# Kernel tuning notes

Hardware: AMD Instinct MI355X
Metric: run time of the kernel (lower is better)

The kernel has to match this reference:

```python
import jax, jax.numpy as jnp
import numpy as np

B, NS, D, H = 1024, 32, 1024, 4096
LN_EPS = 1e-5


def _layer_norm(x, g, b):
    mu = jnp.mean(x, axis=-1, keepdims=True)
    var = jnp.mean(jnp.square(x - mu), axis=-1, keepdims=True)
    return (x - mu) * jax.lax.rsqrt(var + LN_EPS) * g + b


def setup_inputs() -> dict:
    key = jax.random.key(0)
    ks = jax.random.split(key, 12)
    sc = 0.02
    inp = {
        "x": jax.random.normal(ks[0], (B, D), jnp.float32),
        "S": jax.random.normal(ks[1], (B, NS, D), jnp.float32),
        # route_mlp: Linear(2D, D) -> GELU -> Linear(D, NS)
        "w_r1": jax.random.normal(ks[2], (2 * D, D), jnp.float32) * sc,
        "b_r1": jnp.zeros((D,), jnp.float32),
        "w_r2": jax.random.normal(ks[3], (D, NS), jnp.float32) * sc,
        "b_r2": jnp.zeros((NS,), jnp.float32),
        # GRUCell(D, D): gates ordered [r, z, n] as in torch
        "w_ih": jax.random.normal(ks[4], (D, 3 * D), jnp.float32) * sc,
        "w_hh": jax.random.normal(ks[5], (D, 3 * D), jnp.float32) * sc,
        "b_ih": jnp.zeros((3 * D,), jnp.float32),
        "b_hh": jnp.zeros((3 * D,), jnp.float32),
        # slot_proj: Linear(D, D)
        "w_proj": jax.random.normal(ks[6], (D, D), jnp.float32) * sc,
        "b_proj": jnp.zeros((D,), jnp.float32),
        # ln1 / ffn / ln2
        "ln1_g": jnp.ones((D,), jnp.float32),
        "ln1_b": jnp.zeros((D,), jnp.float32),
        "w_f1": jax.random.normal(ks[7], (D, H), jnp.float32) * sc,
        "b_f1": jnp.zeros((H,), jnp.float32),
        "w_f2": jax.random.normal(ks[8], (H, D), jnp.float32) * sc,
        "b_f2": jnp.zeros((D,), jnp.float32),
        "ln2_g": jnp.ones((D,), jnp.float32),
        "ln2_b": jnp.zeros((D,), jnp.float32),
    }
    return inp


def reference(x, S, w_r1, b_r1, w_r2, b_r2, w_ih, w_hh, b_ih, b_hh,
              w_proj, b_proj, ln1_g, ln1_b, w_f1, b_f1, w_f2, b_f2,
              ln2_g, ln2_b):
    tau = 1.0
    # --- context-aware routing ---
    slot_mean = jnp.mean(S, axis=1)                     # [B, D]
    ctx = jnp.concatenate([x, slot_mean], axis=-1)      # [B, 2D]
    h_r = jax.nn.gelu(ctx @ w_r1 + b_r1, approximate=False)
    r_logits = h_r @ w_r2 + b_r2                        # [B, NS]
    alpha = jax.nn.softmax(r_logits / tau, axis=-1)     # [B, NS]

    # --- GRU slot update: input U = alpha * x broadcast over slots ---
    U = alpha[:, :, None] * x[:, None, :]               # [B, NS, D]
    gi = U @ w_ih + b_ih                                # [B, NS, 3D]
    gh = S @ w_hh + b_hh                                # [B, NS, 3D]
    gi_r, gi_z, gi_n = jnp.split(gi, 3, axis=-1)
    gh_r, gh_z, gh_n = jnp.split(gh, 3, axis=-1)
    r = jax.nn.sigmoid(gi_r + gh_r)
    z = jax.nn.sigmoid(gi_z + gh_z)
    n = jnp.tanh(gi_n + r * gh_n)
    S_new = (1.0 - z) * n + z * S                       # [B, NS, D]

    # --- weighted readout (slot_dropout = 0.0) ---
    slot_context = jnp.sum(alpha[:, :, None] * S_new, axis=1)  # [B, D]
    slot_update = slot_context @ w_proj + b_proj
    x_mid = x + slot_update

    # --- FFN + residual + LayerNorms ---
    h = _layer_norm(x_mid, ln1_g, ln1_b)
    ff = jax.nn.gelu(h @ w_f1 + b_f1, approximate=False) @ w_f2 + b_f2
    x_out = _layer_norm(x_mid + ff, ln2_g, ln2_b)
    return (x_out, S_new, alpha)
```

## Files before the change

kernel.cpp:

```cpp
#include <hip/hip_runtime.h>
#include <hip/hip_bf16.h>

#define BB 1024
#define NSLOT 32
#define DD 1024
#define HH 4096

typedef __bf16 bfx8 __attribute__((ext_vector_type(8)));
typedef float f32x4 __attribute__((ext_vector_type(4)));

__device__ __forceinline__ unsigned short f2bfu(float f) {
  union { float f; unsigned u; } v; v.f = f;
  unsigned r = v.u + 0x7fffu + ((v.u >> 16) & 1u);
  return (unsigned short)(r >> 16);
}
__device__ __forceinline__ float bfu2f(unsigned short u) {
  union { unsigned u; float f; } v; v.u = ((unsigned)u) << 16; return v.f;
}
__device__ __forceinline__ float gelu_f(float x) {
  return 0.5f * x * (1.0f + erff(x * 0.70710678118654752f));
}

__device__ __forceinline__ float sigm_fast(float x) {
  return __builtin_amdgcn_rcpf(1.0f + __builtin_amdgcn_exp2f(-1.4426950408889634f * x));
}
__device__ __forceinline__ float tanh_fast(float x) {
  float t = __builtin_amdgcn_exp2f(2.8853900817779268f * x);
  return 1.0f - 2.0f * __builtin_amdgcn_rcpf(1.0f + t);
}

__device__ __forceinline__ void async16(const unsigned short* g, unsigned short* l) {
  __builtin_amdgcn_global_load_lds(
      (const __attribute__((address_space(1))) unsigned int*)g,
      (__attribute__((address_space(3))) unsigned int*)l, 16, 0, 0);
}


__global__ __launch_bounds__(256) void cvt_x_ctx(const float* __restrict__ x,
                                                 unsigned short* __restrict__ ctx) {
  int i = blockIdx.x * 256 + threadIdx.x;
  int b = i >> 8;
  int c4 = (i & 255) * 4;
  float4 v = ((const float4*)(x + (size_t)b * DD))[i & 255];
  ushort4 o; o.x = f2bfu(v.x); o.y = f2bfu(v.y); o.z = f2bfu(v.z); o.w = f2bfu(v.w);
  *(ushort4*)&ctx[(size_t)b * (2 * DD) + c4] = o;
}

__global__ __launch_bounds__(256) void cvt4(const float* __restrict__ in,
                                            unsigned short* __restrict__ out, int n4) {
  int i = blockIdx.x * 256 + threadIdx.x;
  if (i >= n4) return;
  float4 v = ((const float4*)in)[i];
  ushort4 o; o.x = f2bfu(v.x); o.y = f2bfu(v.y); o.z = f2bfu(v.z); o.w = f2bfu(v.w);
  ((ushort4*)out)[i] = o;
}

__global__ __launch_bounds__(256) void slot_mean_k(const unsigned short* __restrict__ Sb,
                                                   unsigned short* __restrict__ ctx) {
  int i = blockIdx.x * 256 + threadIdx.x;
  int b = i >> 10, d = i & 1023;
  const unsigned short* p = Sb + (size_t)b * NSLOT * DD + d;
  float s = 0.f;
  #pragma unroll
  for (int sl = 0; sl < NSLOT; sl++) s += bfu2f(p[sl * DD]);
  ctx[(size_t)b * (2 * DD) + DD + d] = f2bfu(s * (1.0f / NSLOT));
}

__global__ __launch_bounds__(256) void transp(const float* __restrict__ in,
                                              unsigned short* __restrict__ out,
                                              int R, int C) {
  __shared__ float t[32][33];
  int tx = threadIdx.x & 31, ty = threadIdx.x >> 5;
  int c0 = blockIdx.x * 32, r0 = blockIdx.y * 32;
  #pragma unroll
  for (int i = 0; i < 4; i++) {
    int r = r0 + ty * 4 + i;
    t[ty * 4 + i][tx] = in[(size_t)r * C + c0 + tx];
  }
  __syncthreads();
  #pragma unroll
  for (int i = 0; i < 4; i++) {
    int c = c0 + ty * 4 + i;
    out[(size_t)c * R + r0 + tx] = f2bfu(t[tx][ty * 4 + i]);
  }
}

template <int EPI>
__global__ __launch_bounds__(256) void gemm_nt(
    const unsigned short* __restrict__ A, int lda,
    const unsigned short* __restrict__ Bt, int ldb, int K,
    const float* __restrict__ bias,
    const float* __restrict__ add, int ldadd,
    float* __restrict__ outF, unsigned short* __restrict__ outB, int ldout) {
  __shared__ __align__(16) unsigned short lA[2][128 * 32];
  __shared__ __align__(16) unsigned short lB[2][64 * 32];
  const int tid = threadIdx.x;
  const int wave = tid >> 6, lane = tid & 63;
  const int wr = wave >> 1, wc = wave & 1;
  const int q = lane >> 4, l15 = lane & 15;
  const int row0 = blockIdx.y * 128;
  const int col0 = blockIdx.x * 64;
  const int halfA = 128 * 32, halfB = 64 * 32;

  const int lr = lane >> 2, scn = lane & 3;
  const unsigned short* aSrc[2];
  unsigned short* aDst[2];
  #pragma unroll
  for (int j = 0; j < 2; j++) {
    int R0 = (2 * wave + j) * 16;
    int r = R0 + lr;
    int c = scn ^ ((r >> 1) & 3);
    aSrc[j] = A + (size_t)(row0 + r) * lda + c * 8;
    aDst[j] = &lA[0][R0 * 32];
  }
  const unsigned short* bSrc;
  unsigned short* bDst;
  {
    int R0 = wave * 16;
    int r = R0 + lr;
    int c = scn ^ ((r >> 1) & 3);
    bSrc = Bt + (size_t)(col0 + r) * ldb + c * 8;
    bDst = &lB[0][R0 * 32];
  }

  int offA[4];
  #pragma unroll
  for (int m = 0; m < 4; m++) {
    int r = wr * 64 + m * 16 + l15;
    offA[m] = r * 32 + (q ^ ((r >> 1) & 3)) * 8;
  }
  int offB[2];
  #pragma unroll
  for (int n = 0; n < 2; n++) {
    int r = wc * 32 + n * 16 + l15;
    offB[n] = r * 32 + (q ^ ((r >> 1) & 3)) * 8;
  }

  f32x4 acc[4][2];
  #pragma unroll
  for (int m = 0; m < 4; m++)
    #pragma unroll
    for (int n = 0; n < 2; n++) acc[m][n] = (f32x4){0.f, 0.f, 0.f, 0.f};

  const int iters = K >> 6;
  for (int it = 0; it < iters; it++) {
    #pragma unroll
    for (int j = 0; j < 2; j++) {
      async16(aSrc[j], aDst[j]);
      async16(aSrc[j] + 32, aDst[j] + halfA);
      aSrc[j] += 64;
    }
    async16(bSrc, bDst);
    async16(bSrc + 32, bDst + halfB);
    bSrc += 64;
    __syncthreads();
    #pragma unroll
    for (int h = 0; h < 2; h++) {
      bfx8 af[4];
      #pragma unroll
      for (int m = 0; m < 4; m++) af[m] = *(const bfx8*)&lA[h][offA[m]];
      bfx8 bf0 = *(const bfx8*)&lB[h][offB[0]];
      bfx8 bf1 = *(const bfx8*)&lB[h][offB[1]];
      #pragma unroll
      for (int m = 0; m < 4; m++) {
        acc[m][0] = __builtin_amdgcn_mfma_f32_16x16x32_bf16(af[m], bf0, acc[m][0], 0, 0, 0);
        acc[m][1] = __builtin_amdgcn_mfma_f32_16x16x32_bf16(af[m], bf1, acc[m][1], 0, 0, 0);
      }
    }
    __syncthreads();
  }

  #pragma unroll
  for (int m = 0; m < 4; m++) {
    #pragma unroll
    for (int n = 0; n < 2; n++) {
      int gr0 = row0 + wr * 64 + m * 16 + q * 4;
      int gc = col0 + wc * 32 + n * 16 + l15;
      #pragma unroll
      for (int i = 0; i < 4; i++) {
        int gr = gr0 + i;
        float v = acc[m][n][i];
        if (EPI == 0) {
          outF[(size_t)gr * ldout + gc] = v;
        } else if (EPI == 1) {
          float t = gelu_f(v + bias[gc]);
          outB[(size_t)gr * ldout + gc] = f2bfu(t);
        } else {
          outF[(size_t)gr * ldout + gc] = v + bias[gc] + add[(size_t)gr * ldadd + gc];
        }
      }
    }
  }
}

__global__ __launch_bounds__(256, 2) void gru_gemm(
    const unsigned short* __restrict__ Sb, const unsigned short* __restrict__ Whht,
    const float* __restrict__ alpha, const float* __restrict__ xw,
    const float* __restrict__ b_ih, const float* __restrict__ b_hh,
    const float* __restrict__ Sf, float* __restrict__ Snew,
    unsigned short* __restrict__ sc_b) {
  __shared__ __align__(16) unsigned short lA[2][2][128 * 32];
  __shared__ __align__(16) unsigned short lB[2][2][192 * 32];
  const int tid = threadIdx.x;
  const int wave = tid >> 6, lane = tid & 63;
  const int wr = wave >> 1, wc = wave & 1;
  const int q = lane >> 4, l15 = lane & 15;
  const int row0 = blockIdx.y * 128;
  const int col0 = blockIdx.x * 64;

  const int lr = lane >> 2, scn = lane & 3;
  const unsigned short* aSrc[2];
  int aOff[2];
  #pragma unroll
  for (int j = 0; j < 2; j++) {
    int R0 = (2 * wave + j) * 16;
    int r = R0 + lr;
    int c = scn ^ ((r >> 1) & 3);
    aSrc[j] = Sb + (size_t)(row0 + r) * DD + c * 8;
    aOff[j] = R0 * 32;
  }
  const unsigned short* bSrc[3];
  int bOff[3];
  #pragma unroll
  for (int j = 0; j < 3; j++) {
    int R0 = (3 * wave + j) * 16;
    int r = R0 + lr;
    int g = r >> 6, cr = r & 63;
    int c = scn ^ ((r >> 1) & 3);
    bSrc[j] = Whht + ((size_t)g * DD + col0 + cr) * DD + c * 8;
    bOff[j] = R0 * 32;
  }

  int offA[4];
  #pragma unroll
  for (int m = 0; m < 4; m++) {
    int r = wr * 64 + m * 16 + l15;
    offA[m] = r * 32 + (q ^ ((r >> 1) & 3)) * 8;
  }
  int offB[3][2];
  #pragma unroll
  for (int g = 0; g < 3; g++)
    #pragma unroll
    for (int n = 0; n < 2; n++) {
      int r = g * 64 + wc * 32 + n * 16 + l15;
      offB[g][n] = r * 32 + (q ^ ((r >> 1) & 3)) * 8;
    }

  f32x4 acc[3][4][2];
  #pragma unroll
  for (int g = 0; g < 3; g++)
    #pragma unroll
    for (int m = 0; m < 4; m++)
      #pragma unroll
      for (int n = 0; n < 2; n++) acc[g][m][n] = (f32x4){0.f, 0.f, 0.f, 0.f};

#define STAGE(BUF)                                                          \
  {                                                                         \
    _Pragma("unroll")                                                       \
    for (int j = 0; j < 2; j++) {                                           \
      async16(aSrc[j], &lA[BUF][0][aOff[j]]);                               \
      async16(aSrc[j] + 32, &lA[BUF][1][aOff[j]]);                          \
      aSrc[j] += 64;                                                        \
    }                                                                       \
    _Pragma("unroll")                                                       \
    for (int j = 0; j < 3; j++) {                                           \
      async16(bSrc[j], &lB[BUF][0][bOff[j]]);                               \
      async16(bSrc[j] + 32, &lB[BUF][1][bOff[j]]);                          \
      bSrc[j] += 64;                                                        \
    }                                                                       \
  }

#define COMPUTE(BUF)                                                        \
  {                                                                         \
    _Pragma("unroll")                                                       \
    for (int h = 0; h < 2; h++) {                                           \
      bfx8 af[4];                                                           \
      _Pragma("unroll")                                                     \
      for (int m = 0; m < 4; m++) af[m] = *(const bfx8*)&lA[BUF][h][offA[m]]; \
      _Pragma("unroll")                                                     \
      for (int g = 0; g < 3; g++) {                                         \
        bfx8 bf0 = *(const bfx8*)&lB[BUF][h][offB[g][0]];                   \
        bfx8 bf1 = *(const bfx8*)&lB[BUF][h][offB[g][1]];                   \
        _Pragma("unroll")                                                   \
        for (int m = 0; m < 4; m++) {                                       \
          acc[g][m][0] = __builtin_amdgcn_mfma_f32_16x16x32_bf16(af[m], bf0, acc[g][m][0], 0, 0, 0); \
          acc[g][m][1] = __builtin_amdgcn_mfma_f32_16x16x32_bf16(af[m], bf1, acc[g][m][1], 0, 0, 0); \
        }                                                                   \
      }                                                                     \
    }                                                                       \
  }

#define WAIT_VM10 asm volatile("s_waitcnt vmcnt(10)" ::: "memory")
#define WAIT_VM0  asm volatile("s_waitcnt vmcnt(0)" ::: "memory")
#define WAIT_LGKM asm volatile("s_waitcnt lgkmcnt(0)" ::: "memory")
#define BAR __builtin_amdgcn_s_barrier()

  STAGE(0);
  for (int t = 0; t < 8; t++) {
    STAGE(1);
    WAIT_VM10; BAR;
    COMPUTE(0);
    WAIT_LGKM; BAR;
    if (t < 7) {
      STAGE(0);
      WAIT_VM10;
    } else {
      WAIT_VM0;
    }
    BAR;
    COMPUTE(1);
    if (t < 7) { WAIT_LGKM; BAR; }
  }

#undef STAGE
#undef COMPUTE
#undef WAIT_VM10
#undef WAIT_VM0
#undef WAIT_LGKM
#undef BAR

  float sfv[4][2][4];
  float av[4][4];
  #pragma unroll
  for (int m = 0; m < 4; m++) {
    #pragma unroll
    for (int i = 0; i < 4; i++) {
      int gr = row0 + wr * 64 + m * 16 + q * 4 + i;
      av[m][i] = alpha[gr];
      const float* sfr = Sf + (size_t)gr * DD;
      #pragma unroll
      for (int n = 0; n < 2; n++)
        sfv[m][n][i] = sfr[col0 + wc * 32 + n * 16 + l15];
    }
  }

  float scp[2][2] = {{0.f, 0.f}, {0.f, 0.f}};
  #pragma unroll
  for (int m = 0; m < 4; m++) {
    #pragma unroll
    for (int i = 0; i < 4; i++) {
      int gr = row0 + wr * 64 + m * 16 + q * 4 + i;
      float a = av[m][i];
      const float* xwr = xw + (size_t)(gr >> 5) * (3 * DD);
      float* orow = Snew + (size_t)gr * DD;
      #pragma unroll
      for (int n = 0; n < 2; n++) {
        int gc = col0 + wc * 32 + n * 16 + l15;
        float ghr = acc[0][m][n][i] + b_hh[gc];
        float ghz = acc[1][m][n][i] + b_hh[gc + DD];
        float ghn = acc[2][m][n][i] + b_hh[gc + 2 * DD];
        float r = sigm_fast(a * xwr[gc] + b_ih[gc] + ghr);
        float z = sigm_fast(a * xwr[gc + DD] + b_ih[gc + DD] + ghz);
        float nn = tanh_fast(a * xwr[gc + 2 * DD] + b_ih[gc + 2 * DD] + r * ghn);
        float sv = (1.0f - z) * nn + z * sfv[m][n][i];
        orow[gc] = sv;
        scp[m >> 1][n] += a * sv;
      }
    }
  }
  #pragma unroll
  for (int bh = 0; bh < 2; bh++)
    #pragma unroll
    for (int n = 0; n < 2; n++) {
      float v = scp[bh][n];
      v += __shfl_xor(v, 16);
      v += __shfl_xor(v, 32);
      if (q == 0) {
        int batch = (row0 >> 5) + wr * 2 + bh;
        int gc = col0 + wc * 32 + n * 16 + l15;
        sc_b[(size_t)batch * DD + gc] = f2bfu(v);
      }
    }
}

__global__ __launch_bounds__(256) void route_softmax(
    const unsigned short* __restrict__ h_r, const float* __restrict__ w_r2,
    const float* __restrict__ b_r2, float* __restrict__ alpha_out) {
  int b = blockIdx.x;
  int n = threadIdx.x & 31, c = threadIdx.x >> 5;
  __shared__ float part[8][32];
  __shared__ float logits[32];
  const unsigned short* hr = h_r + (size_t)b * DD;
  float s = 0.f;
  for (int i = 0; i < 128; i++) {
    int k = c * 128 + i;
    s += bfu2f(hr[k]) * w_r2[k * NSLOT + n];
  }
  part[c][n] = s;
  __syncthreads();
  if (threadIdx.x < 32) {
    float t = b_r2[n];
    #pragma unroll
    for (int cc = 0; cc < 8; cc++) t += part[cc][n];
    logits[n] = t;
  }
  __syncthreads();
  if (threadIdx.x < 32) {
    float mx = -1e30f;
    #pragma unroll
    for (int j = 0; j < 32; j++) mx = fmaxf(mx, logits[j]);
    float den = 0.f;
    #pragma unroll
    for (int j = 0; j < 32; j++) den += expf(logits[j] - mx);
    alpha_out[(size_t)b * NSLOT + n] = expf(logits[n] - mx) / den;
  }
}

template <int OUT_BF>
__global__ __launch_bounds__(256) void ln_k(const float* __restrict__ in,
                                            const float* __restrict__ gw,
                                            const float* __restrict__ bw,
                                            float* __restrict__ outF,
                                            unsigned short* __restrict__ outB) {
  int b = blockIdx.x;
  int tid = threadIdx.x;
  float4 v = ((const float4*)(in + (size_t)b * DD))[tid];
  float s = v.x + v.y + v.z + v.w;
  float s2 = v.x * v.x + v.y * v.y + v.z * v.z + v.w * v.w;
  #pragma unroll
  for (int o = 32; o > 0; o >>= 1) { s += __shfl_down(s, o); s2 += __shfl_down(s2, o); }
  __shared__ float as1[4], as2[4];
  int wave = tid >> 6, lane = tid & 63;
  if (lane == 0) { as1[wave] = s; as2[wave] = s2; }
  __syncthreads();
  float t1 = as1[0] + as1[1] + as1[2] + as1[3];
  float t2 = as2[0] + as2[1] + as2[2] + as2[3];
  float mu = t1 * (1.0f / DD);
  float var = t2 * (1.0f / DD) - mu * mu;
  float rstd = rsqrtf(var + 1e-5f);
  int d = tid * 4;
  float o0 = (v.x - mu) * rstd * gw[d] + bw[d];
  float o1 = (v.y - mu) * rstd * gw[d + 1] + bw[d + 1];
  float o2 = (v.z - mu) * rstd * gw[d + 2] + bw[d + 2];
  float o3 = (v.w - mu) * rstd * gw[d + 3] + bw[d + 3];
  if (OUT_BF) {
    ushort4 o; o.x = f2bfu(o0); o.y = f2bfu(o1); o.z = f2bfu(o2); o.w = f2bfu(o3);
    *(ushort4*)&outB[(size_t)b * DD + d] = o;
  } else {
    float4 o; o.x = o0; o.y = o1; o.z = o2; o.w = o3;
    *(float4*)&outF[(size_t)b * DD + d] = o;
  }
}

extern "C" void kernel_launch(void* const* d_in, const int* in_sizes, int n_in,
                              void* d_out, int out_size, void* d_ws, size_t ws_size,
                              hipStream_t stream) {
  const float* x      = (const float*)d_in[0];
  const float* S      = (const float*)d_in[1];
  const float* w_r1   = (const float*)d_in[2];
  const float* b_r1   = (const float*)d_in[3];
  const float* w_r2   = (const float*)d_in[4];
  const float* b_r2   = (const float*)d_in[5];
  const float* w_ih   = (const float*)d_in[6];
  const float* w_hh   = (const float*)d_in[7];
  const float* b_ih   = (const float*)d_in[8];
  const float* b_hh   = (const float*)d_in[9];
  const float* w_proj = (const float*)d_in[10];
  const float* b_proj = (const float*)d_in[11];
  const float* ln1_g  = (const float*)d_in[12];
  const float* ln1_b  = (const float*)d_in[13];
  const float* w_f1   = (const float*)d_in[14];
  const float* b_f1   = (const float*)d_in[15];
  const float* w_f2   = (const float*)d_in[16];
  const float* b_f2   = (const float*)d_in[17];
  const float* ln2_g  = (const float*)d_in[18];
  const float* ln2_b  = (const float*)d_in[19];

  float* out_x = (float*)d_out;
  float* out_S = out_x + (size_t)BB * DD;
  float* out_a = out_S + (size_t)BB * NSLOT * DD;

  char* ws = (char*)d_ws;
  unsigned short* ctx    = (unsigned short*)(ws + 0);
  unsigned short* w_r1t  = (unsigned short*)(ws + 4194304);
  unsigned short* w_iht  = (unsigned short*)(ws + 8388608);
  unsigned short* w_hht  = (unsigned short*)(ws + 14680064);
  unsigned short* w_projt= (unsigned short*)(ws + 20971520);
  unsigned short* w_f1t  = (unsigned short*)(ws + 23068672);
  unsigned short* w_f2t  = (unsigned short*)(ws + 31457280);
  unsigned short* h_r    = (unsigned short*)(ws + 39845888);
  float*          xw     = (float*)(ws + 41943040);
  unsigned short* Sb     = (unsigned short*)(ws + 54525952);
  unsigned short* sc_b   = (unsigned short*)(ws + 0);
  float*          x_mid  = (float*)(ws + 41943040);
  unsigned short* h_ln   = (unsigned short*)(ws + 46137344);
  float*          pre2   = (float*)(ws + 48234496);
  unsigned short* ff1    = (unsigned short*)(ws + 54525952);

  dim3 blk(256);
  cvt_x_ctx<<<1024, blk, 0, stream>>>(x, ctx);
  cvt4<<<32768, blk, 0, stream>>>(S, Sb, (BB * NSLOT * DD) / 4);
  slot_mean_k<<<4096, blk, 0, stream>>>(Sb, ctx);
  transp<<<dim3(32, 64), blk, 0, stream>>>(w_r1, w_r1t, 2 * DD, DD);
  transp<<<dim3(96, 32), blk, 0, stream>>>(w_ih, w_iht, DD, 3 * DD);
  transp<<<dim3(96, 32), blk, 0, stream>>>(w_hh, w_hht, DD, 3 * DD);
  transp<<<dim3(32, 32), blk, 0, stream>>>(w_proj, w_projt, DD, DD);
  transp<<<dim3(128, 32), blk, 0, stream>>>(w_f1, w_f1t, DD, HH);
  transp<<<dim3(32, 128), blk, 0, stream>>>(w_f2, w_f2t, HH, DD);

  gemm_nt<1><<<dim3(16, 8), blk, 0, stream>>>(ctx, 2 * DD, w_r1t, 2 * DD, 2 * DD,
                                              b_r1, nullptr, 0, nullptr, h_r, DD);
  route_softmax<<<1024, blk, 0, stream>>>(h_r, w_r2, b_r2, out_a);

  gemm_nt<0><<<dim3(48, 8), blk, 0, stream>>>(ctx, 2 * DD, w_iht, DD, DD,
                                              nullptr, nullptr, 0, xw, nullptr, 3 * DD);

  gru_gemm<<<dim3(16, 256), blk, 0, stream>>>(Sb, w_hht, out_a, xw, b_ih, b_hh, S,
                                              out_S, sc_b);

  gemm_nt<2><<<dim3(16, 8), blk, 0, stream>>>(sc_b, DD, w_projt, DD, DD,
                                              b_proj, x, DD, x_mid, nullptr, DD);

  ln_k<1><<<1024, blk, 0, stream>>>(x_mid, ln1_g, ln1_b, nullptr, h_ln);
  gemm_nt<1><<<dim3(64, 8), blk, 0, stream>>>(h_ln, DD, w_f1t, DD, DD,
                                              b_f1, nullptr, 0, nullptr, ff1, HH);
  gemm_nt<2><<<dim3(16, 8), blk, 0, stream>>>(ff1, HH, w_f2t, HH, HH,
                                              b_f2, x_mid, DD, pre2, nullptr, DD);
  ln_k<0><<<1024, blk, 0, stream>>>(pre2, ln2_g, ln2_b, out_x, nullptr);
}
```

Before: 759.5 us.

## Double-buffer LDS in bf16 GEMM to overlap async loads with MFMA

Adds a second LDS stage to the NT GEMM so the global-to-LDS async copies for the next K-tile are issued before computing the current one. Partial vmcnt waits and explicit barriers replace the per-iteration full syncs. This is meant to hide global load latency behind MFMA work, at the cost of doubling LDS use per block (which may lower occupancy). It also assumes K is a multiple of 128.

```diff
diff --git a/kernel.cpp b/kernel.cpp
--- a/kernel.cpp
+++ b/kernel.cpp
@@ -92,35 +92,34 @@
     const float* __restrict__ bias,
     const float* __restrict__ add, int ldadd,
     float* __restrict__ outF, unsigned short* __restrict__ outB, int ldout) {
-  __shared__ __align__(16) unsigned short lA[2][128 * 32];
-  __shared__ __align__(16) unsigned short lB[2][64 * 32];
+  __shared__ __align__(16) unsigned short lA[2][2][128 * 32];
+  __shared__ __align__(16) unsigned short lB[2][2][64 * 32];
   const int tid = threadIdx.x;
   const int wave = tid >> 6, lane = tid & 63;
   const int wr = wave >> 1, wc = wave & 1;
   const int q = lane >> 4, l15 = lane & 15;
   const int row0 = blockIdx.y * 128;
   const int col0 = blockIdx.x * 64;
-  const int halfA = 128 * 32, halfB = 64 * 32;
 
   const int lr = lane >> 2, scn = lane & 3;
   const unsigned short* aSrc[2];
-  unsigned short* aDst[2];
+  int aOff[2];
   #pragma unroll
   for (int j = 0; j < 2; j++) {
     int R0 = (2 * wave + j) * 16;
     int r = R0 + lr;
     int c = scn ^ ((r >> 1) & 3);
     aSrc[j] = A + (size_t)(row0 + r) * lda + c * 8;
-    aDst[j] = &lA[0][R0 * 32];
+    aOff[j] = R0 * 32;
   }
   const unsigned short* bSrc;
-  unsigned short* bDst;
+  int bOff0;
   {
     int R0 = wave * 16;
     int r = R0 + lr;
     int c = scn ^ ((r >> 1) & 3);
     bSrc = Bt + (size_t)(col0 + r) * ldb + c * 8;
-    bDst = &lB[0][R0 * 32];
+    bOff0 = R0 * 32;
   }
 
   int offA[4];
@@ -142,33 +141,65 @@
     #pragma unroll
     for (int n = 0; n < 2; n++) acc[m][n] = (f32x4){0.f, 0.f, 0.f, 0.f};
 
-  const int iters = K >> 6;
-  for (int it = 0; it < iters; it++) {
-    #pragma unroll
-    for (int j = 0; j < 2; j++) {
-      async16(aSrc[j], aDst[j]);
-      async16(aSrc[j] + 32, aDst[j] + halfA);
-      aSrc[j] += 64;
-    }
-    async16(bSrc, bDst);
-    async16(bSrc + 32, bDst + halfB);
-    bSrc += 64;
-    __syncthreads();
-    #pragma unroll
-    for (int h = 0; h < 2; h++) {
-      bfx8 af[4];
-      #pragma unroll
-      for (int m = 0; m < 4; m++) af[m] = *(const bfx8*)&lA[h][offA[m]];
-      bfx8 bf0 = *(const bfx8*)&lB[h][offB[0]];
-      bfx8 bf1 = *(const bfx8*)&lB[h][offB[1]];
-      #pragma unroll
-      for (int m = 0; m < 4; m++) {
-        acc[m][0] = __builtin_amdgcn_mfma_f32_16x16x32_bf16(af[m], bf0, acc[m][0], 0, 0, 0);
-        acc[m][1] = __builtin_amdgcn_mfma_f32_16x16x32_bf16(af[m], bf1, acc[m][1], 0, 0, 0);
-      }
-    }
-    __syncthreads();
-  }
+#define GSTAGE(BUF)                                                         \
+  {                                                                         \
+    _Pragma("unroll")                                                       \
+    for (int j = 0; j < 2; j++) {                                           \
+      async16(aSrc[j], &lA[BUF][0][aOff[j]]);                               \
+      async16(aSrc[j] + 32, &lA[BUF][1][aOff[j]]);                          \
+      aSrc[j] += 64;                                                        \
+    }                                                                       \
+    async16(bSrc, &lB[BUF][0][bOff0]);                                      \
+    async16(bSrc + 32, &lB[BUF][1][bOff0]);                                 \
+    bSrc += 64;                                                             \
+  }
+
+#define GCOMPUTE(BUF)                                                       \
+  {                                                                         \
+    _Pragma("unroll")                                                       \
+    for (int h = 0; h < 2; h++) {                                           \
+      bfx8 af[4];                                                           \
+      _Pragma("unroll")                                                     \
+      for (int m = 0; m < 4; m++) af[m] = *(const bfx8*)&lA[BUF][h][offA[m]]; \
+      bfx8 bf0 = *(const bfx8*)&lB[BUF][h][offB[0]];                        \
+      bfx8 bf1 = *(const bfx8*)&lB[BUF][h][offB[1]];                        \
+      _Pragma("unroll")                                                     \
+      for (int m = 0; m < 4; m++) {                                         \
+        acc[m][0] = __builtin_amdgcn_mfma_f32_16x16x32_bf16(af[m], bf0, acc[m][0], 0, 0, 0); \
+        acc[m][1] = __builtin_amdgcn_mfma_f32_16x16x32_bf16(af[m], bf1, acc[m][1], 0, 0, 0); \
+      }                                                                     \
+    }                                                                       \
+  }
+
+#define GWAIT_VM6 asm volatile("s_waitcnt vmcnt(6)" ::: "memory")
+#define GWAIT_VM0 asm volatile("s_waitcnt vmcnt(0)" ::: "memory")
+#define GWAIT_LGKM asm volatile("s_waitcnt lgkmcnt(0)" ::: "memory")
+#define GBAR __builtin_amdgcn_s_barrier()
+
+  const int pairs = K >> 7;
+  GSTAGE(0);
+  for (int t = 0; t < pairs; t++) {
+    GSTAGE(1);
+    GWAIT_VM6; GBAR;
+    GCOMPUTE(0);
+    GWAIT_LGKM; GBAR;
+    if (t < pairs - 1) {
+      GSTAGE(0);
+      GWAIT_VM6;
+    } else {
+      GWAIT_VM0;
+    }
+    GBAR;
+    GCOMPUTE(1);
+    if (t < pairs - 1) { GWAIT_LGKM; GBAR; }
+  }
+
+#undef GSTAGE
+#undef GCOMPUTE
+#undef GWAIT_VM6
+#undef GWAIT_VM0
+#undef GWAIT_LGKM
+#undef GBAR
 
   #pragma unroll
   for (int m = 0; m < 4; m++) {
```

Measured after the change: 752.6 us. No clear change (-0.9%).
